# Kernel tuning notes

Measured on AMD Instinct MI355X. Metric: run time of the kernel, lower is better.

Reference implementation:

```python
import jax, jax.numpy as jnp
import numpy as np

D = 1024      # d_model
H = 8         # heads
DH = D // H
L = 12        # layers
E = 4         # experts
F = 2048      # dim_feedforward
NCLS = 10
SPARSITY = 0.5
EPS = 1e-5
B, S = 4, 512


def _xavier(key, shape):
    fan_in, fan_out = shape[-1], shape[-2] if len(shape) > 1 else shape[-1]
    scale = jnp.sqrt(2.0 / (fan_in + fan_out))
    return jax.random.normal(key, shape, jnp.float32) * scale


def setup_inputs() -> dict:
    key = jax.random.key(0)
    ks = jax.random.split(key, 16)
    return {
        "x": jax.random.normal(ks[0], (B, S, D), jnp.float32),
        "pos": jax.random.normal(ks[1], (1, 512, D), jnp.float32) * 0.02,
        # stacked per-layer transformer params
        "Wqkv": _xavier(ks[2], (L, 3 * D, D)), "bqkv": jnp.zeros((L, 3 * D), jnp.float32),
        "Wo": _xavier(ks[3], (L, D, D)),       "bo": jnp.zeros((L, D), jnp.float32),
        "ln1_s": jnp.ones((L, D), jnp.float32), "ln1_b": jnp.zeros((L, D), jnp.float32),
        "W1": _xavier(ks[4], (L, F, D)), "b1": jnp.zeros((L, F), jnp.float32),
        "W2": _xavier(ks[5], (L, D, F)), "b2": jnp.zeros((L, D), jnp.float32),
        "ln2_s": jnp.ones((L, D), jnp.float32), "ln2_b": jnp.zeros((L, D), jnp.float32),
        # shared gate / experts / classifier
        "Wg": _xavier(ks[6], (E, D)), "bg": jnp.zeros((E,), jnp.float32),
        "We": _xavier(ks[7], (E, D, D)), "be": jnp.zeros((E, D), jnp.float32),
        "Wf": _xavier(ks[8], (NCLS, D)), "bf": jnp.zeros((NCLS,), jnp.float32),
    }


def _layernorm(x, s, b):
    m = jnp.mean(x, axis=-1, keepdims=True)
    v = jnp.mean(jnp.square(x - m), axis=-1, keepdims=True)
    return (x - m) * jax.lax.rsqrt(v + EPS) * s + b


def _forward(x, pos, Wqkv, bqkv, Wo, bo, ln1_s, ln1_b, W1, b1, W2, b2,
             ln2_s, ln2_b, Wg, bg, We, be, Wf, bf):
    Bx, Sx, _ = x.shape
    x = x + pos[:, :Sx, :]
    for l in range(L):
        # --- self-attention (post-norm TransformerEncoderLayer, eval/no-dropout) ---
        qkv = x @ Wqkv[l].T + bqkv[l]                      # [B,S,3D]
        q, k, v = jnp.split(qkv, 3, axis=-1)
        q = q.reshape(Bx, Sx, H, DH).transpose(0, 2, 1, 3)  # bhsd
        k = k.reshape(Bx, Sx, H, DH).transpose(0, 2, 1, 3)
        v = v.reshape(Bx, Sx, H, DH).transpose(0, 2, 1, 3)
        attn = jax.nn.softmax(jnp.einsum('bhqd,bhkd->bhqk', q, k) / jnp.sqrt(jnp.float32(DH)), axis=-1)
        o = jnp.einsum('bhqk,bhkd->bhqd', attn, v).transpose(0, 2, 1, 3).reshape(Bx, Sx, D)
        o = o @ Wo[l].T + bo[l]
        x = _layernorm(x + o, ln1_s[l], ln1_b[l])
        # --- ffn (exact gelu) ---
        h = jax.nn.gelu(x @ W1[l].T + b1[l], approximate=False) @ W2[l].T + b2[l]
        x = _layernorm(x + h, ln2_s[l], ln2_b[l])
        # --- top-2 gated MoE (shared gate/experts across layers) ---
        gs = jax.nn.softmax(x @ Wg.T + bg, axis=-1)         # [B,S,E]
        vals, idx = jax.lax.top_k(gs, 2)                    # [B,S,2]
        all_out = jnp.einsum('bsd,eod->bseo', x, We) + be   # [B,S,E,D]
        sel = jnp.take_along_axis(all_out, idx[..., None], axis=2)  # [B,S,2,D]
        expert_out = jnp.sum(sel * vals[..., None], axis=2)
        x = x * (1.0 - SPARSITY) + expert_out * SPARSITY
    return x[:, -1, :] @ Wf.T + bf                          # [B,10]


def reference(x, pos, Wqkv, bqkv, Wo, bo, ln1_s, ln1_b, W1, b1, W2, b2,
              ln2_s, ln2_b, Wg, bg, We, be, Wf, bf):
    return _forward(x, pos, Wqkv, bqkv, Wo, bo, ln1_s, ln1_b, W1, b1, W2, b2,
                    ln2_s, ln2_b, Wg, bg, We, be, Wf, bf)
```

## Files before the change

### kernel.cpp

```cpp
#include <hip/hip_runtime.h>
#include <math.h>

#define D     1024
#define NH    8
#define DHD   128
#define NL    12
#define NE    4
#define FF    2048
#define NCLS  10
#define BB    4
#define SS    512
#define TT    (BB*SS)
#define EPSV  1e-5f
#define SPARS 0.5f

typedef __attribute__((ext_vector_type(8))) short bf16x8;
typedef __attribute__((ext_vector_type(4))) float f32x4;
typedef unsigned short ushortT;

__device__ __forceinline__ ushortT f2bf(float f) {
    unsigned u = __float_as_uint(f);
    u += 0x7FFF + ((u >> 16) & 1);
    return (ushortT)(u >> 16);
}
__device__ __forceinline__ float bf2f(ushortT h) {
    return __uint_as_float(((unsigned)h) << 16);
}

#define LDP 40

template<int MODE, int SK, int ACT>
__global__ __launch_bounds__(256)
void gemm_mfma(const ushortT* __restrict__ A, const float* __restrict__ Bw,
               const float* __restrict__ bias, void* __restrict__ Cv,
               int M, int N, int Ktot, int Klen, long eBw, long eBias, long eC)
{
    const int z = blockIdx.z;
    int koff = 0;
    float* Cf = nullptr; ushortT* Ch = nullptr;
    if constexpr (SK > 1) {
        koff = z * Klen;
        Cf = (float*)Cv + (size_t)z * M * N;
    } else {
        Bw   += (size_t)z * eBw;
        bias += (size_t)z * eBias;
        if constexpr (MODE == 0) Ch = (ushortT*)Cv + (size_t)z * eC;
        else                     Cf = (float*)Cv   + (size_t)z * eC;
    }

    __shared__ ushortT Asl[128 * LDP];
    __shared__ ushortT Bsl[128 * LDP];

    const int tid  = threadIdx.x;
    const int wave = tid >> 6, lane = tid & 63;
    const int wm = (wave >> 1) * 64;
    const int wn = (wave & 1) * 64;
    const int fr = lane & 15;
    const int fq = lane >> 4;

    const int m0 = blockIdx.y * 128;
    const int n0 = blockIdx.x * 128;

    const int arow = tid >> 1;
    const int akc  = (tid & 1) * 2;
    const ushortT* Ag = A + (size_t)(m0 + arow) * Ktot + koff;
    const int srow = tid >> 3;
    const int scb  = tid & 7;
    const float* Bg = Bw + (size_t)(n0 + srow) * Ktot + koff + scb * 4;

    f32x4 acc[4][4] = {};

    for (int k0 = 0; k0 < Klen; k0 += 32) {
        bf16x8 av8[2];
        float4 bv[4];
        #pragma unroll
        for (int u = 0; u < 2; ++u)
            av8[u] = *reinterpret_cast<const bf16x8*>(Ag + k0 + (akc + u) * 8);
        #pragma unroll
        for (int p = 0; p < 4; ++p)
            bv[p] = *reinterpret_cast<const float4*>(Bg + (size_t)(32*p) * Ktot + k0);
        __syncthreads();
        #pragma unroll
        for (int u = 0; u < 2; ++u)
            *reinterpret_cast<bf16x8*>(&Asl[arow*LDP + (akc + u)*8]) = av8[u];
        #pragma unroll
        for (int p = 0; p < 4; ++p) {
            const int r = srow + 32*p;
            ushort4 b4; b4.x=f2bf(bv[p].x); b4.y=f2bf(bv[p].y); b4.z=f2bf(bv[p].z); b4.w=f2bf(bv[p].w);
            *reinterpret_cast<ushort4*>(&Bsl[r*LDP + scb*4]) = b4;
        }
        __syncthreads();

        bf16x8 af[4], bf_[4];
        #pragma unroll
        for (int i = 0; i < 4; ++i) {
            af[i]  = *reinterpret_cast<const bf16x8*>(&Asl[(wm + i*16 + fr)*LDP + fq*8]);
            bf_[i] = *reinterpret_cast<const bf16x8*>(&Bsl[(wn + i*16 + fr)*LDP + fq*8]);
        }
        #pragma unroll
        for (int i = 0; i < 4; ++i)
            #pragma unroll
            for (int j = 0; j < 4; ++j)
                acc[i][j] = __builtin_amdgcn_mfma_f32_16x16x32_bf16(af[i], bf_[j], acc[i][j], 0, 0, 0);
    }

    #pragma unroll
    for (int j = 0; j < 4; ++j) {
        const int n = n0 + wn + j*16 + fr;
        float bb = 0.f;
        if constexpr (SK == 1) bb = bias[n];
        #pragma unroll
        for (int i = 0; i < 4; ++i) {
            const int mbase = m0 + wm + i*16 + fq*4;
            #pragma unroll
            for (int r = 0; r < 4; ++r) {
                float u = acc[i][j][r] + bb;
                if constexpr (SK == 1 && ACT == 1)
                    u = 0.5f*u*(1.0f + erff(u*0.70710678118654752f));
                if constexpr (SK > 1)       Cf[(size_t)(mbase + r) * N + n] = u;
                else if constexpr (MODE==0) Ch[(size_t)(mbase + r) * N + n] = f2bf(u);
                else                        Cf[(size_t)(mbase + r) * N + n] = u;
            }
        }
    }
}

__global__ __launch_bounds__(256)
void kv_prep(const float* __restrict__ qkv, ushortT* __restrict__ Kb, ushortT* __restrict__ Vt)
{
    __shared__ ushortT T[64*136];
    const int tid = threadIdx.x;
    const int st = blockIdx.x, bh = blockIdx.y;
    const int b = bh >> 3, h = bh & 7;
    const float* base = qkv + (size_t)(b*SS + st*64)*3*D + h*DHD;

    #pragma unroll
    for (int p = 0; p < 4; ++p) {
        const int row = (tid >> 4) + 16*p;
        const int colb = (tid & 15) * 8;
        {
            const float* src = base + (size_t)row*3*D + D + colb;
            float f[8];
            *reinterpret_cast<float4*>(f)   = *reinterpret_cast<const float4*>(src);
            *reinterpret_cast<float4*>(f+4) = *reinterpret_cast<const float4*>(src+4);
            bf16x8 u;
            #pragma unroll
            for (int e = 0; e < 8; ++e) ((ushortT*)&u)[e] = f2bf(f[e]);
            *reinterpret_cast<bf16x8*>(&Kb[((size_t)bh*SS + st*64 + row)*DHD + colb]) = u;
        }
        {
            const float* src = base + (size_t)row*3*D + 2*D + colb;
            float f[8];
            *reinterpret_cast<float4*>(f)   = *reinterpret_cast<const float4*>(src);
            *reinterpret_cast<float4*>(f+4) = *reinterpret_cast<const float4*>(src+4);
            #pragma unroll
            for (int e = 0; e < 8; ++e) T[row*136 + colb + e] = f2bf(f[e]);
        }
    }
    __syncthreads();
    #pragma unroll
    for (int p = 0; p < 4; ++p) {
        const int d  = (tid >> 3) + 32*p;
        const int sb = (tid & 7) * 8;
        bf16x8 u;
        #pragma unroll
        for (int e = 0; e < 8; ++e) ((ushortT*)&u)[e] = T[(sb + e)*136 + d];
        *reinterpret_cast<bf16x8*>(&Vt[((size_t)bh*DHD + d)*SS + st*64 + sb]) = u;
    }
}

#define KLP 136
#define VLP 72
#define PLP 72

__global__ __launch_bounds__(256)
void attn_mfma(const float* __restrict__ qkv, const ushortT* __restrict__ Kb,
               const ushortT* __restrict__ Vt, ushortT* __restrict__ o16)
{
    __shared__ ushortT Kl[64*KLP];
    __shared__ ushortT Vl[128*VLP];
    __shared__ ushortT Pl[4*16*PLP];

    const int tid = threadIdx.x;
    const int w = tid >> 6, lane = tid & 63;
    const int g = lane >> 4, c = lane & 15;
    const int bh = blockIdx.y;
    const int b = bh >> 3, h = bh & 7;
    const int q0 = blockIdx.x*64 + w*16;
    ushortT* Pw = Pl + w*16*PLP;

    bf16x8 qhi[4], qlo[4];
    const float scale = 0.08838834764831845f;
    {
        const float* Qrow = qkv + (size_t)(b*SS + q0 + c)*3*D + h*DHD;
        #pragma unroll
        for (int db = 0; db < 4; ++db) {
            float f[8];
            *reinterpret_cast<float4*>(f)   = *reinterpret_cast<const float4*>(Qrow + db*32 + g*8);
            *reinterpret_cast<float4*>(f+4) = *reinterpret_cast<const float4*>(Qrow + db*32 + g*8 + 4);
            #pragma unroll
            for (int e = 0; e < 8; ++e) {
                const float fs = f[e]*scale;
                const ushortT hi = f2bf(fs);
                ((ushortT*)&qhi[db])[e] = hi;
                ((ushortT*)&qlo[db])[e] = f2bf(fs - bf2f(hi));
            }
        }
    }

    const ushortT* Kg = Kb + (size_t)bh*SS*DHD;
    const ushortT* Vg = Vt + (size_t)bh*DHD*SS;

    float m_r[4], l_r[4];
    #pragma unroll
    for (int r = 0; r < 4; ++r) { m_r[r] = -1e30f; l_r[r] = 0.f; }
    f32x4 oacc[8] = {};

    for (int kt = 0; kt < SS/64; ++kt) {
        __syncthreads();
        #pragma unroll
        for (int p = 0; p < 4; ++p) {
            const int row = (tid >> 4) + 16*p;
            const int colb = (tid & 15)*8;
            bf16x8 u = *reinterpret_cast<const bf16x8*>(&Kg[(size_t)(kt*64 + row)*DHD + colb]);
            *reinterpret_cast<bf16x8*>(&Kl[row*KLP + colb]) = u;
        }
        #pragma unroll
        for (int p = 0; p < 4; ++p) {
            const int dr = (tid >> 3) + 32*p;
            const int sb = (tid & 7)*8;
            bf16x8 u = *reinterpret_cast<const bf16x8*>(&Vg[(size_t)dr*SS + kt*64 + sb]);
            *reinterpret_cast<bf16x8*>(&Vl[dr*VLP + sb]) = u;
        }
        __syncthreads();

        f32x4 s[4] = {};
        #pragma unroll
        for (int db = 0; db < 4; ++db) {
            bf16x8 kf[4];
            #pragma unroll
            for (int kb = 0; kb < 4; ++kb)
                kf[kb] = *reinterpret_cast<const bf16x8*>(&Kl[(kb*16 + c)*KLP + db*32 + g*8]);
            #pragma unroll
            for (int kb = 0; kb < 4; ++kb) {
                s[kb] = __builtin_amdgcn_mfma_f32_16x16x32_bf16(qhi[db], kf[kb], s[kb], 0, 0, 0);
                s[kb] = __builtin_amdgcn_mfma_f32_16x16x32_bf16(qlo[db], kf[kb], s[kb], 0, 0, 0);
            }
        }

        float tmax[4];
        #pragma unroll
        for (int r = 0; r < 4; ++r)
            tmax[r] = fmaxf(fmaxf(s[0][r], s[1][r]), fmaxf(s[2][r], s[3][r]));
        #pragma unroll
        for (int off = 1; off < 16; off <<= 1)
            #pragma unroll
            for (int r = 0; r < 4; ++r)
                tmax[r] = fmaxf(tmax[r], __shfl_xor(tmax[r], off));
        float mn[4], corr[4];
        #pragma unroll
        for (int r = 0; r < 4; ++r) {
            mn[r] = fmaxf(m_r[r], tmax[r]);
            corr[r] = __expf(m_r[r] - mn[r]);
            m_r[r] = mn[r];
        }
        float tsum[4] = {0.f, 0.f, 0.f, 0.f};
        #pragma unroll
        for (int kb = 0; kb < 4; ++kb)
            #pragma unroll
            for (int r = 0; r < 4; ++r) {
                const float p = __expf(s[kb][r] - mn[r]);
                s[kb][r] = p;
                tsum[r] += p;
            }
        #pragma unroll
        for (int off = 1; off < 16; off <<= 1)
            #pragma unroll
            for (int r = 0; r < 4; ++r)
                tsum[r] += __shfl_xor(tsum[r], off);
        #pragma unroll
        for (int r = 0; r < 4; ++r) l_r[r] = l_r[r]*corr[r] + tsum[r];
        #pragma unroll
        for (int df = 0; df < 8; ++df)
            #pragma unroll
            for (int r = 0; r < 4; ++r)
                oacc[df][r] *= corr[r];

        #pragma unroll
        for (int kb = 0; kb < 4; ++kb)
            #pragma unroll
            for (int r = 0; r < 4; ++r)
                Pw[(g*4 + r)*PLP + kb*16 + c] = f2bf(s[kb][r]);

        #pragma unroll
        for (int kk = 0; kk < 2; ++kk) {
            bf16x8 pa = *reinterpret_cast<const bf16x8*>(&Pw[c*PLP + kk*32 + g*8]);
            #pragma unroll
            for (int df = 0; df < 8; ++df) {
                bf16x8 vb = *reinterpret_cast<const bf16x8*>(&Vl[(df*16 + c)*VLP + kk*32 + g*8]);
                oacc[df] = __builtin_amdgcn_mfma_f32_16x16x32_bf16(pa, vb, oacc[df], 0, 0, 0);
            }
        }
    }

    #pragma unroll
    for (int r = 0; r < 4; ++r) {
        const float inv = 1.0f / l_r[r];
        ushortT* orow = o16 + (size_t)(b*SS + q0 + g*4 + r)*D + h*DHD + c;
        #pragma unroll
        for (int df = 0; df < 8; ++df)
            orow[df*16] = f2bf(oacc[df][r] * inv);
    }
}

template<int SK, int GATE>
__global__ __launch_bounds__(256)
void add_ln_r(const float* __restrict__ xin, const float* __restrict__ P,
              const float* __restrict__ dbias,
              const float* __restrict__ gs, const float* __restrict__ gb,
              float* __restrict__ x32, ushortT* __restrict__ x16,
              const float* __restrict__ Wg, const float* __restrict__ bg,
              float* __restrict__ gv, int* __restrict__ gi)
{
    const int row = blockIdx.x, tid = threadIdx.x;
    const size_t off = (size_t)row*D + tid*4;
    float4 a = *reinterpret_cast<const float4*>(xin + off);
    float d0, d1, d2, d3;
    {
        float4 bvd = *reinterpret_cast<const float4*>(dbias + tid*4);
        d0 = bvd.x; d1 = bvd.y; d2 = bvd.z; d3 = bvd.w;
    }
    #pragma unroll
    for (int s = 0; s < SK; ++s) {
        float4 pv = *reinterpret_cast<const float4*>(P + (size_t)s*TT*D + off);
        d0 += pv.x; d1 += pv.y; d2 += pv.z; d3 += pv.w;
    }
    float v0=a.x+d0, v1=a.y+d1, v2=a.z+d2, v3=a.w+d3;
    __shared__ float red[2][4];
    float s = v0+v1+v2+v3;
    #pragma unroll
    for (int o = 32; o; o >>= 1) s += __shfl_xor(s, o, 64);
    if ((tid & 63) == 0) red[0][tid>>6] = s;
    __syncthreads();
    const float mean = (red[0][0]+red[0][1]+red[0][2]+red[0][3]) * (1.0f/D);
    v0-=mean; v1-=mean; v2-=mean; v3-=mean;
    float qv = v0*v0+v1*v1+v2*v2+v3*v3;
    #pragma unroll
    for (int o = 32; o; o >>= 1) qv += __shfl_xor(qv, o, 64);
    if ((tid & 63) == 0) red[1][tid>>6] = qv;
    __syncthreads();
    const float var = (red[1][0]+red[1][1]+red[1][2]+red[1][3]) * (1.0f/D);
    const float rstd = rsqrtf(var + EPSV);
    float4 sv = *reinterpret_cast<const float4*>(gs + tid*4);
    float4 bv = *reinterpret_cast<const float4*>(gb + tid*4);
    float ov[4];
    ov[0] = v0*rstd*sv.x + bv.x;
    ov[1] = v1*rstd*sv.y + bv.y;
    ov[2] = v2*rstd*sv.z + bv.z;
    ov[3] = v3*rstd*sv.w + bv.w;
    float4 o4; o4.x=ov[0]; o4.y=ov[1]; o4.z=ov[2]; o4.w=ov[3];
    *reinterpret_cast<float4*>(x32 + off) = o4;
    ushort4 h4; h4.x=f2bf(ov[0]); h4.y=f2bf(ov[1]); h4.z=f2bf(ov[2]); h4.w=f2bf(ov[3]);
    *reinterpret_cast<ushort4*>(x16 + off) = h4;

    if constexpr (GATE) {
        float p[4] = {0.f, 0.f, 0.f, 0.f};
        #pragma unroll
        for (int e = 0; e < 4; ++e) {
            const float* wr = Wg + (size_t)e*D + tid*4;
            p[e] = ov[0]*wr[0] + ov[1]*wr[1] + ov[2]*wr[2] + ov[3]*wr[3];
        }
        #pragma unroll
        for (int o = 32; o; o >>= 1) {
            p[0] += __shfl_xor(p[0], o, 64); p[1] += __shfl_xor(p[1], o, 64);
            p[2] += __shfl_xor(p[2], o, 64); p[3] += __shfl_xor(p[3], o, 64);
        }
        __shared__ float gred[4][4];
        if ((tid & 63) == 0) {
            const int w = tid>>6;
            gred[w][0]=p[0]; gred[w][1]=p[1]; gred[w][2]=p[2]; gred[w][3]=p[3];
        }
        __syncthreads();
        if (tid == 0) {
            float g[4];
            #pragma unroll
            for (int e = 0; e < 4; ++e) g[e] = gred[0][e]+gred[1][e]+gred[2][e]+gred[3][e] + bg[e];
            const float mx = fmaxf(fmaxf(g[0],g[1]), fmaxf(g[2],g[3]));
            float ssum = 0.f;
            #pragma unroll
            for (int e = 0; e < 4; ++e) { g[e] = __expf(g[e]-mx); ssum += g[e]; }
            const float inv = 1.0f/ssum;
            #pragma unroll
            for (int e = 0; e < 4; ++e) g[e] *= inv;
            int i0 = 0;
            for (int e = 1; e < 4; ++e) if (g[e] > g[i0]) i0 = e;
            int i1 = (i0 == 0) ? 1 : 0;
            for (int e = 0; e < 4; ++e) if (e != i0 && g[e] > g[i1]) i1 = e;
            gv[row*2]   = g[i0]; gv[row*2+1] = g[i1];
            gi[row*2]   = i0;    gi[row*2+1] = i1;
        }
    }
}

__global__ __launch_bounds__(256)
void moe_combine(float* __restrict__ x, ushortT* __restrict__ x16,
                 const float* __restrict__ eo,
                 const float* __restrict__ gv, const int* __restrict__ gi)
{
    const size_t i = (size_t)blockIdx.x*256 + threadIdx.x;
    const int t = (int)(i >> 10);
    const float w0 = gv[t*2]*SPARS, w1 = gv[t*2+1]*SPARS;
    const size_t TD = (size_t)TT*D;
    const float e0 = eo[(size_t)gi[t*2]*TD + i];
    const float e1 = eo[(size_t)gi[t*2+1]*TD + i];
    const float r = x[i]*(1.0f-SPARS) + w0*e0 + w1*e1;
    x[i] = r;
    x16[i] = f2bf(r);
}

__global__ __launch_bounds__(256)
void addpos(const float* __restrict__ xin, const float* __restrict__ pos,
            float* __restrict__ xo, ushortT* __restrict__ x16)
{
    const size_t i = (size_t)blockIdx.x*256 + threadIdx.x;
    const float r = xin[i] + pos[i & ((size_t)SS*D - 1)];
    xo[i] = r;
    x16[i] = f2bf(r);
}

__global__ __launch_bounds__(64)
void final_kernel(const float* __restrict__ x, const float* __restrict__ Wf,
                  const float* __restrict__ bf, float* __restrict__ out)
{
    const int b = blockIdx.x / NCLS, n = blockIdx.x % NCLS;
    const float* xr = x + ((size_t)b*SS + SS-1)*D;
    const int tid = threadIdx.x;
    float s = 0.f;
    for (int d = tid; d < D; d += 64) s += xr[d]*Wf[(size_t)n*D + d];
    #pragma unroll
    for (int o = 32; o; o >>= 1) s += __shfl_xor(s, o, 64);
    if (tid == 0) out[b*NCLS + n] = s + bf[n];
}

extern "C" void kernel_launch(void* const* d_in, const int* in_sizes, int n_in,
                              void* d_out, int out_size, void* d_ws, size_t ws_size,
                              hipStream_t stream)
{
    const float* x_in = (const float*)d_in[0];
    const float* pos  = (const float*)d_in[1];
    const float* Wqkv = (const float*)d_in[2];
    const float* bqkv = (const float*)d_in[3];
    const float* Wo   = (const float*)d_in[4];
    const float* bo   = (const float*)d_in[5];
    const float* ln1s = (const float*)d_in[6];
    const float* ln1b = (const float*)d_in[7];
    const float* W1   = (const float*)d_in[8];
    const float* b1   = (const float*)d_in[9];
    const float* W2   = (const float*)d_in[10];
    const float* b2   = (const float*)d_in[11];
    const float* ln2s = (const float*)d_in[12];
    const float* ln2b = (const float*)d_in[13];
    const float* Wg   = (const float*)d_in[14];
    const float* bg   = (const float*)d_in[15];
    const float* We   = (const float*)d_in[16];
    const float* be   = (const float*)d_in[17];
    const float* Wf   = (const float*)d_in[18];
    const float* bf   = (const float*)d_in[19];
    float* out = (float*)d_out;

    float* ws     = (float*)d_ws;
    float*   xbuf  = ws;
    ushortT* xb16  = (ushortT*)(xbuf + (size_t)TT*D);
    ushortT* ob16  = xb16 + (size_t)TT*D;
    float*   scratch = (float*)(ob16 + (size_t)TT*D);
    ushortT* hb16  = (ushortT*)(scratch + (size_t)8*1024*1024/4*4);
    hb16 = (ushortT*)(scratch + (size_t)TT*D*4);
    float*   gv    = (float*)(hb16 + (size_t)TT*FF);
    int*     gi    = (int*)(gv + (size_t)TT*2);
    float*   qkvbuf = scratch;
    ushortT* Kb     = (ushortT*)(qkvbuf + (size_t)TT*3*D);
    ushortT* Vt     = Kb + (size_t)BB*NH*SS*DHD;
    float*   parts  = scratch;
    float*   ebuf   = scratch;

    const dim3 blk(256);
    addpos<<<dim3(TT*D/256), blk, 0, stream>>>(x_in, pos, xbuf, xb16);

    for (int l = 0; l < NL; ++l) {
        gemm_mfma<1,1,0><<<dim3(3*D/128, TT/128, 1), blk, 0, stream>>>(
            xb16, Wqkv + (size_t)l*3*D*D, bqkv + (size_t)l*3*D, qkvbuf,
            TT, 3*D, D, D, 0, 0, 0);
        kv_prep<<<dim3(SS/64, BB*NH), blk, 0, stream>>>(qkvbuf, Kb, Vt);
        attn_mfma<<<dim3(SS/64, BB*NH), blk, 0, stream>>>(qkvbuf, Kb, Vt, ob16);
        gemm_mfma<1,4,0><<<dim3(D/128, TT/128, 4), blk, 0, stream>>>(
            ob16, Wo + (size_t)l*D*D, bo, parts, TT, D, D, D/4, 0, 0, 0);
        add_ln_r<4,0><<<dim3(TT), blk, 0, stream>>>(
            xbuf, parts, bo + (size_t)l*D, ln1s + (size_t)l*D, ln1b + (size_t)l*D,
            xbuf, xb16, nullptr, nullptr, nullptr, nullptr);
        gemm_mfma<0,1,1><<<dim3(FF/128, TT/128, 1), blk, 0, stream>>>(
            xb16, W1 + (size_t)l*FF*D, b1 + (size_t)l*FF, hb16, TT, FF, D, D, 0, 0, 0);
        gemm_mfma<1,4,0><<<dim3(D/128, TT/128, 4), blk, 0, stream>>>(
            hb16, W2 + (size_t)l*D*FF, b2, parts, TT, D, FF, FF/4, 0, 0, 0);
        add_ln_r<4,1><<<dim3(TT), blk, 0, stream>>>(
            xbuf, parts, b2 + (size_t)l*D, ln2s + (size_t)l*D, ln2b + (size_t)l*D,
            xbuf, xb16, Wg, bg, gv, gi);
        gemm_mfma<1,1,0><<<dim3(D/128, TT/128, NE), blk, 0, stream>>>(
            xb16, We, be, ebuf, TT, D, D, D, (long)D*D, (long)D, (long)TT*D);
        moe_combine<<<dim3(TT*D/256), blk, 0, stream>>>(xbuf, xb16, ebuf, gv, gi);
    }
    final_kernel<<<dim3(BB*NCLS), dim3(64), 0, stream>>>(xbuf, Wf, bf, out);
}
```

Measured before the change: 2.871 ms.

## Route MoE tokens to experts sparsely, fuse QKV split epilogue, prefetch GEMM tiles

The MoE expert GEMM now runs only over the tokens routed to each expert. The gate kernel builds per-expert token lists with atomics, the GEMM gathers A rows through those lists and exits early for empty tiles, and the combine step reads outputs by slot. This roughly halves expert FLOPs versus computing all four experts for every token. The QKV GEMM epilogue writes Q as fp32, K as bf16 and V transposed directly, which removes the kv_prep kernel and its fp32 round trip. The GEMM main loop also prefetches the next k-tile into registers before the MFMA work. Risks are atomic-ordering nondeterminism in the slot order and extra uncoalesced V-transpose stores.

```diff
diff --git a/kernel.cpp b/kernel.cpp
--- a/kernel.cpp
+++ b/kernel.cpp
@@ -29,13 +29,25 @@
 
 #define LDP 40
 
-template<int MODE, int SK, int ACT>
+template<int MODE, int SK, int ACT, int EPI>
 __global__ __launch_bounds__(256)
 void gemm_mfma(const ushortT* __restrict__ A, const float* __restrict__ Bw,
                const float* __restrict__ bias, void* __restrict__ Cv,
-               int M, int N, int Ktot, int Klen, long eBw, long eBias, long eC)
+               int M, int N, int Ktot, int Klen,
+               long eBw, long eBias, long eC,
+               float* __restrict__ qp, ushortT* __restrict__ kp, ushortT* __restrict__ vp,
+               const int* __restrict__ slotTok, const int* __restrict__ cnt)
 {
     const int z = blockIdx.z;
+    const int m0 = blockIdx.y * 128;
+    const int n0 = blockIdx.x * 128;
+
+    int cntE = 0;
+    if constexpr (EPI == 2) {
+        cntE = cnt[z];
+        if (m0 >= cntE) return;
+    }
+
     int koff = 0;
     float* Cf = nullptr; ushortT* Ch = nullptr;
     if constexpr (SK > 1) {
@@ -58,50 +70,61 @@
     const int fr = lane & 15;
     const int fq = lane >> 4;
 
-    const int m0 = blockIdx.y * 128;
-    const int n0 = blockIdx.x * 128;
-
     const int arow = tid >> 1;
-    const int akc  = (tid & 1) * 2;
-    const ushortT* Ag = A + (size_t)(m0 + arow) * Ktot + koff;
+    const int akc  = (tid & 1) * 16;
+    const ushortT* Ag;
+    if constexpr (EPI == 2) {
+        const int rsl = m0 + arow;
+        const int tok = (rsl < cntE) ? slotTok[(size_t)z*TT + rsl] : 0;
+        Ag = A + (size_t)tok * Ktot;
+    } else {
+        Ag = A + (size_t)(m0 + arow) * Ktot + koff;
+    }
     const int srow = tid >> 3;
     const int scb  = tid & 7;
     const float* Bg = Bw + (size_t)(n0 + srow) * Ktot + koff + scb * 4;
 
     f32x4 acc[4][4] = {};
+    bf16x8 av8[2];
+    float4 bv[4];
+
+    av8[0] = *reinterpret_cast<const bf16x8*>(Ag + akc);
+    av8[1] = *reinterpret_cast<const bf16x8*>(Ag + akc + 8);
+    #pragma unroll
+    for (int p = 0; p < 4; ++p)
+        bv[p] = *reinterpret_cast<const float4*>(Bg + (size_t)(32*p) * Ktot);
 
     for (int k0 = 0; k0 < Klen; k0 += 32) {
-        bf16x8 av8[2];
-        float4 bv[4];
-        #pragma unroll
-        for (int u = 0; u < 2; ++u)
-            av8[u] = *reinterpret_cast<const bf16x8*>(Ag + k0 + (akc + u) * 8);
-        #pragma unroll
-        for (int p = 0; p < 4; ++p)
-            bv[p] = *reinterpret_cast<const float4*>(Bg + (size_t)(32*p) * Ktot + k0);
         __syncthreads();
-        #pragma unroll
-        for (int u = 0; u < 2; ++u)
-            *reinterpret_cast<bf16x8*>(&Asl[arow*LDP + (akc + u)*8]) = av8[u];
+        *reinterpret_cast<bf16x8*>(&Asl[arow*LDP + akc])     = av8[0];
+        *reinterpret_cast<bf16x8*>(&Asl[arow*LDP + akc + 8]) = av8[1];
         #pragma unroll
         for (int p = 0; p < 4; ++p) {
-            const int r = srow + 32*p;
             ushort4 b4; b4.x=f2bf(bv[p].x); b4.y=f2bf(bv[p].y); b4.z=f2bf(bv[p].z); b4.w=f2bf(bv[p].w);
-            *reinterpret_cast<ushort4*>(&Bsl[r*LDP + scb*4]) = b4;
+            *reinterpret_cast<ushort4*>(&Bsl[(srow + 32*p)*LDP + scb*4]) = b4;
         }
         __syncthreads();
 
-        bf16x8 af[4], bf_[4];
+        const int kn = k0 + 32;
+        if (kn < Klen) {
+            av8[0] = *reinterpret_cast<const bf16x8*>(Ag + kn + akc);
+            av8[1] = *reinterpret_cast<const bf16x8*>(Ag + kn + akc + 8);
+            #pragma unroll
+            for (int p = 0; p < 4; ++p)
+                bv[p] = *reinterpret_cast<const float4*>(Bg + (size_t)(32*p) * Ktot + kn);
+        }
+
+        bf16x8 af[4], bfr[4];
         #pragma unroll
         for (int i = 0; i < 4; ++i) {
             af[i]  = *reinterpret_cast<const bf16x8*>(&Asl[(wm + i*16 + fr)*LDP + fq*8]);
-            bf_[i] = *reinterpret_cast<const bf16x8*>(&Bsl[(wn + i*16 + fr)*LDP + fq*8]);
+            bfr[i] = *reinterpret_cast<const bf16x8*>(&Bsl[(wn + i*16 + fr)*LDP + fq*8]);
         }
         #pragma unroll
         for (int i = 0; i < 4; ++i)
             #pragma unroll
             for (int j = 0; j < 4; ++j)
-                acc[i][j] = __builtin_amdgcn_mfma_f32_16x16x32_bf16(af[i], bf_[j], acc[i][j], 0, 0, 0);
+                acc[i][j] = __builtin_amdgcn_mfma_f32_16x16x32_bf16(af[i], bfr[j], acc[i][j], 0, 0, 0);
     }
 
     #pragma unroll
@@ -111,61 +134,46 @@
         if constexpr (SK == 1) bb = bias[n];
         #pragma unroll
         for (int i = 0; i < 4; ++i) {
-            const int mbase = m0 + wm + i*16 + fq*4;
-            #pragma unroll
-            for (int r = 0; r < 4; ++r) {
-                float u = acc[i][j][r] + bb;
-                if constexpr (SK == 1 && ACT == 1)
-                    u = 0.5f*u*(1.0f + erff(u*0.70710678118654752f));
-                if constexpr (SK > 1)       Cf[(size_t)(mbase + r) * N + n] = u;
-                else if constexpr (MODE==0) Ch[(size_t)(mbase + r) * N + n] = f2bf(u);
-                else                        Cf[(size_t)(mbase + r) * N + n] = u;
+            const int mb = m0 + wm + i*16 + fq*4;
+            if constexpr (EPI == 1) {
+                if (n0 < D) {
+                    #pragma unroll
+                    for (int r = 0; r < 4; ++r)
+                        qp[(size_t)(mb + r)*D + n] = acc[i][j][r] + bb;
+                } else if (n0 < 2*D) {
+                    #pragma unroll
+                    for (int r = 0; r < 4; ++r)
+                        kp[(size_t)(mb + r)*D + (n - D)] = f2bf(acc[i][j][r] + bb);
+                } else {
+                    const int nv = n - 2*D, hv = nv >> 7, dv = nv & 127;
+                    const int b = mb >> 9, s = mb & 511;
+                    ushort4 pk;
+                    pk.x = f2bf(acc[i][j][0] + bb);
+                    pk.y = f2bf(acc[i][j][1] + bb);
+                    pk.z = f2bf(acc[i][j][2] + bb);
+                    pk.w = f2bf(acc[i][j][3] + bb);
+                    *reinterpret_cast<ushort4*>(vp + (((size_t)b*NH + hv)*DHD + dv)*SS + s) = pk;
+                }
+            } else if constexpr (SK > 1) {
+                #pragma unroll
+                for (int r = 0; r < 4; ++r)
+                    Cf[(size_t)(mb + r) * N + n] = acc[i][j][r];
+            } else if constexpr (MODE == 0) {
+                #pragma unroll
+                for (int r = 0; r < 4; ++r) {
+                    float u = acc[i][j][r] + bb;
+                    if constexpr (ACT == 1) u = 0.5f*u*(1.0f + erff(u*0.70710678118654752f));
+                    Ch[(size_t)(mb + r) * N + n] = f2bf(u);
+                }
+            } else {
+                #pragma unroll
+                for (int r = 0; r < 4; ++r) {
+                    float u = acc[i][j][r] + bb;
+                    if constexpr (ACT == 1) u = 0.5f*u*(1.0f + erff(u*0.70710678118654752f));
+                    Cf[(size_t)(mb + r) * N + n] = u;
+                }
             }
         }
-    }
-}
-
-__global__ __launch_bounds__(256)
-void kv_prep(const float* __restrict__ qkv, ushortT* __restrict__ Kb, ushortT* __restrict__ Vt)
-{
-    __shared__ ushortT T[64*136];
-    const int tid = threadIdx.x;
-    const int st = blockIdx.x, bh = blockIdx.y;
-    const int b = bh >> 3, h = bh & 7;
-    const float* base = qkv + (size_t)(b*SS + st*64)*3*D + h*DHD;
-
-    #pragma unroll
-    for (int p = 0; p < 4; ++p) {
-        const int row = (tid >> 4) + 16*p;
-        const int colb = (tid & 15) * 8;
-        {
-            const float* src = base + (size_t)row*3*D + D + colb;
-            float f[8];
-            *reinterpret_cast<float4*>(f)   = *reinterpret_cast<const float4*>(src);
-            *reinterpret_cast<float4*>(f+4) = *reinterpret_cast<const float4*>(src+4);
-            bf16x8 u;
-            #pragma unroll
-            for (int e = 0; e < 8; ++e) ((ushortT*)&u)[e] = f2bf(f[e]);
-            *reinterpret_cast<bf16x8*>(&Kb[((size_t)bh*SS + st*64 + row)*DHD + colb]) = u;
-        }
-        {
-            const float* src = base + (size_t)row*3*D + 2*D + colb;
-            float f[8];
-            *reinterpret_cast<float4*>(f)   = *reinterpret_cast<const float4*>(src);
-            *reinterpret_cast<float4*>(f+4) = *reinterpret_cast<const float4*>(src+4);
-            #pragma unroll
-            for (int e = 0; e < 8; ++e) T[row*136 + colb + e] = f2bf(f[e]);
-        }
-    }
-    __syncthreads();
-    #pragma unroll
-    for (int p = 0; p < 4; ++p) {
-        const int d  = (tid >> 3) + 32*p;
-        const int sb = (tid & 7) * 8;
-        bf16x8 u;
-        #pragma unroll
-        for (int e = 0; e < 8; ++e) ((ushortT*)&u)[e] = T[(sb + e)*136 + d];
-        *reinterpret_cast<bf16x8*>(&Vt[((size_t)bh*DHD + d)*SS + st*64 + sb]) = u;
     }
 }
 
@@ -174,7 +182,7 @@
 #define PLP 72
 
 __global__ __launch_bounds__(256)
-void attn_mfma(const float* __restrict__ qkv, const ushortT* __restrict__ Kb,
+void attn_mfma(const float* __restrict__ Qb, const ushortT* __restrict__ Kbf,
                const ushortT* __restrict__ Vt, ushortT* __restrict__ o16)
 {
     __shared__ ushortT Kl[64*KLP];
@@ -192,7 +200,7 @@
     bf16x8 qhi[4], qlo[4];
     const float scale = 0.08838834764831845f;
     {
-        const float* Qrow = qkv + (size_t)(b*SS + q0 + c)*3*D + h*DHD;
+        const float* Qrow = Qb + (size_t)(b*SS + q0 + c)*D + h*DHD;
         #pragma unroll
         for (int db = 0; db < 4; ++db) {
             float f[8];
@@ -208,7 +216,7 @@
         }
     }
 
-    const ushortT* Kg = Kb + (size_t)bh*SS*DHD;
+    const ushortT* Kg = Kbf + (size_t)b*SS*D + h*DHD;
     const ushortT* Vg = Vt + (size_t)bh*DHD*SS;
 
     float m_r[4], l_r[4];
@@ -222,7 +230,7 @@
         for (int p = 0; p < 4; ++p) {
             const int row = (tid >> 4) + 16*p;
             const int colb = (tid & 15)*8;
-            bf16x8 u = *reinterpret_cast<const bf16x8*>(&Kg[(size_t)(kt*64 + row)*DHD + colb]);
+            bf16x8 u = *reinterpret_cast<const bf16x8*>(&Kg[(size_t)(kt*64 + row)*D + colb]);
             *reinterpret_cast<bf16x8*>(&Kl[row*KLP + colb]) = u;
         }
         #pragma unroll
@@ -320,7 +328,8 @@
               const float* __restrict__ gs, const float* __restrict__ gb,
               float* __restrict__ x32, ushortT* __restrict__ x16,
               const float* __restrict__ Wg, const float* __restrict__ bg,
-              float* __restrict__ gv, int* __restrict__ gi)
+              float* __restrict__ gv, int* __restrict__ slotTok,
+              int* __restrict__ tokSlot, int* __restrict__ cntL)
 {
     const int row = blockIdx.x, tid = threadIdx.x;
     const size_t off = (size_t)row*D + tid*4;
@@ -397,7 +406,12 @@
             int i1 = (i0 == 0) ? 1 : 0;
             for (int e = 0; e < 4; ++e) if (e != i0 && g[e] > g[i1]) i1 = e;
             gv[row*2]   = g[i0]; gv[row*2+1] = g[i1];
-            gi[row*2]   = i0;    gi[row*2+1] = i1;
+            const int p0 = atomicAdd(&cntL[i0], 1);
+            slotTok[i0*TT + p0] = row;
+            const int p1 = atomicAdd(&cntL[i1], 1);
+            slotTok[i1*TT + p1] = row;
+            tokSlot[row*2]   = i0*TT + p0;
+            tokSlot[row*2+1] = i1*TT + p1;
         }
     }
 }
@@ -405,14 +419,14 @@
 __global__ __launch_bounds__(256)
 void moe_combine(float* __restrict__ x, ushortT* __restrict__ x16,
                  const float* __restrict__ eo,
-                 const float* __restrict__ gv, const int* __restrict__ gi)
+                 const float* __restrict__ gv, const int* __restrict__ tokSlot)
 {
     const size_t i = (size_t)blockIdx.x*256 + threadIdx.x;
     const int t = (int)(i >> 10);
+    const int col = (int)(i & 1023);
     const float w0 = gv[t*2]*SPARS, w1 = gv[t*2+1]*SPARS;
-    const size_t TD = (size_t)TT*D;
-    const float e0 = eo[(size_t)gi[t*2]*TD + i];
-    const float e1 = eo[(size_t)gi[t*2+1]*TD + i];
+    const float e0 = eo[(size_t)tokSlot[t*2]  *D + col];
+    const float e1 = eo[(size_t)tokSlot[t*2+1]*D + col];
     const float r = x[i]*(1.0f-SPARS) + w0*e0 + w1*e1;
     x[i] = r;
     x16[i] = f2bf(r);
@@ -426,6 +440,12 @@
     const float r = xin[i] + pos[i & ((size_t)SS*D - 1)];
     xo[i] = r;
     x16[i] = f2bf(r);
+}
+
+__global__ __launch_bounds__(64)
+void zero_cnt(int* __restrict__ cnt)
+{
+    if (threadIdx.x < NL*NE) cnt[threadIdx.x] = 0;
 }
 
 __global__ __launch_bounds__(64)
@@ -468,45 +488,49 @@
     const float* bf   = (const float*)d_in[19];
     float* out = (float*)d_out;
 
-    float* ws     = (float*)d_ws;
-    float*   xbuf  = ws;
-    ushortT* xb16  = (ushortT*)(xbuf + (size_t)TT*D);
-    ushortT* ob16  = xb16 + (size_t)TT*D;
-    float*   scratch = (float*)(ob16 + (size_t)TT*D);
-    ushortT* hb16  = (ushortT*)(scratch + (size_t)8*1024*1024/4*4);
-    hb16 = (ushortT*)(scratch + (size_t)TT*D*4);
-    float*   gv    = (float*)(hb16 + (size_t)TT*FF);
-    int*     gi    = (int*)(gv + (size_t)TT*2);
-    float*   qkvbuf = scratch;
-    ushortT* Kb     = (ushortT*)(qkvbuf + (size_t)TT*3*D);
-    ushortT* Vt     = Kb + (size_t)BB*NH*SS*DHD;
-    float*   parts  = scratch;
-    float*   ebuf   = scratch;
+    char* w = (char*)d_ws;
+    float*   xbuf    = (float*)w;            w += (size_t)TT*D*4;
+    ushortT* xb16    = (ushortT*)w;          w += (size_t)TT*D*2;
+    ushortT* ob16    = (ushortT*)w;          w += (size_t)TT*D*2;
+    ushortT* hb16    = (ushortT*)w;          w += (size_t)TT*FF*2;
+    float*   Qbuf    = (float*)w;            w += (size_t)TT*D*4;
+    ushortT* Kbf     = (ushortT*)w;          w += (size_t)TT*D*2;
+    ushortT* Vt      = (ushortT*)w;          w += (size_t)TT*D*2;
+    float*   parts   = (float*)w;            w += (size_t)4*TT*D*4;
+    float*   slotOut = (float*)w;            w += (size_t)NE*TT*D*4;
+    float*   gv      = (float*)w;            w += (size_t)TT*2*4;
+    int*     tokSlot = (int*)w;              w += (size_t)TT*2*4;
+    int*     slotTok = (int*)w;              w += (size_t)NE*TT*4;
+    int*     cnt     = (int*)w;              w += (size_t)NL*NE*4;
 
     const dim3 blk(256);
+    zero_cnt<<<dim3(1), dim3(64), 0, stream>>>(cnt);
     addpos<<<dim3(TT*D/256), blk, 0, stream>>>(x_in, pos, xbuf, xb16);
 
     for (int l = 0; l < NL; ++l) {
-        gemm_mfma<1,1,0><<<dim3(3*D/128, TT/128, 1), blk, 0, stream>>>(
-            xb16, Wqkv + (size_t)l*3*D*D, bqkv + (size_t)l*3*D, qkvbuf,
-            TT, 3*D, D, D, 0, 0, 0);
-        kv_prep<<<dim3(SS/64, BB*NH), blk, 0, stream>>>(qkvbuf, Kb, Vt);
-        attn_mfma<<<dim3(SS/64, BB*NH), blk, 0, stream>>>(qkvbuf, Kb, Vt, ob16);
-        gemm_mfma<1,4,0><<<dim3(D/128, TT/128, 4), blk, 0, stream>>>(
-            ob16, Wo + (size_t)l*D*D, bo, parts, TT, D, D, D/4, 0, 0, 0);
+        gemm_mfma<1,1,0,1><<<dim3(3*D/128, TT/128, 1), blk, 0, stream>>>(
+            xb16, Wqkv + (size_t)l*3*D*D, bqkv + (size_t)l*3*D, nullptr,
+            TT, 3*D, D, D, 0, 0, 0, Qbuf, Kbf, Vt, nullptr, nullptr);
+        attn_mfma<<<dim3(SS/64, BB*NH), blk, 0, stream>>>(Qbuf, Kbf, Vt, ob16);
+        gemm_mfma<1,4,0,0><<<dim3(D/128, TT/128, 4), blk, 0, stream>>>(
+            ob16, Wo + (size_t)l*D*D, bo, parts, TT, D, D, D/4, 0, 0, 0,
+            nullptr, nullptr, nullptr, nullptr, nullptr);
         add_ln_r<4,0><<<dim3(TT), blk, 0, stream>>>(
             xbuf, parts, bo + (size_t)l*D, ln1s + (size_t)l*D, ln1b + (size_t)l*D,
-            xbuf, xb16, nullptr, nullptr, nullptr, nullptr);
-        gemm_mfma<0,1,1><<<dim3(FF/128, TT/128, 1), blk, 0, stream>>>(
-            xb16, W1 + (size_t)l*FF*D, b1 + (size_t)l*FF, hb16, TT, FF, D, D, 0, 0, 0);
-        gemm_mfma<1,4,0><<<dim3(D/128, TT/128, 4), blk, 0, stream>>>(
-            hb16, W2 + (size_t)l*D*FF, b2, parts, TT, D, FF, FF/4, 0, 0, 0);
+            xbuf, xb16, nullptr, nullptr, nullptr, nullptr, nullptr, nullptr);
+        gemm_mfma<0,1,1,0><<<dim3(FF/128, TT/128, 1), blk, 0, stream>>>(
+            xb16, W1 + (size_t)l*FF*D, b1 + (size_t)l*FF, hb16, TT, FF, D, D, 0, 0, 0,
+            nullptr, nullptr, nullptr, nullptr, nullptr);
+        gemm_mfma<1,4,0,0><<<dim3(D/128, TT/128, 4), blk, 0, stream>>>(
+            hb16, W2 + (size_t)l*D*FF, b2, parts, TT, D, FF, FF/4, 0, 0, 0,
+            nullptr, nullptr, nullptr, nullptr, nullptr);
         add_ln_r<4,1><<<dim3(TT), blk, 0, stream>>>(
             xbuf, parts, b2 + (size_t)l*D, ln2s + (size_t)l*D, ln2b + (size_t)l*D,
-            xbuf, xb16, Wg, bg, gv, gi);
-        gemm_mfma<1,1,0><<<dim3(D/128, TT/128, NE), blk, 0, stream>>>(
-            xb16, We, be, ebuf, TT, D, D, D, (long)D*D, (long)D, (long)TT*D);
-        moe_combine<<<dim3(TT*D/256), blk, 0, stream>>>(xbuf, xb16, ebuf, gv, gi);
+            xbuf, xb16, Wg, bg, gv, slotTok, tokSlot, cnt + l*NE);
+        gemm_mfma<1,1,0,2><<<dim3(D/128, TT/128, NE), blk, 0, stream>>>(
+            xb16, We, be, slotOut, TT, D, D, D, (long)D*D, (long)D, (long)TT*D,
+            nullptr, nullptr, nullptr, slotTok, cnt + l*NE);
+        moe_combine<<<dim3(TT*D/256), blk, 0, stream>>>(xbuf, xb16, slotOut, gv, tokSlot);
     }
     final_kernel<<<dim3(BB*NCLS), dim3(64), 0, stream>>>(xbuf, Wf, bf, out);
 }
```

Result: slower. 3.203 ms (+11.6%).
